# Performance work log

Hardware: AMD Instinct MI355X
Metric: run time of the kernel (lower is better)

The kernel has to match this reference:

```python
import jax, jax.numpy as jnp
import numpy as np

HIDDEN = 1024
NUM_EXPERTS = 8
TOP_K = 2
BATCH, SEQ = 4, 2048


def setup_inputs() -> dict:
    key = jax.random.key(0)
    ks = jax.random.split(key, 7)
    s = 0.02
    x = jax.random.normal(ks[0], (BATCH, SEQ, HIDDEN), dtype=jnp.float32)
    Wr = jax.random.normal(ks[1], (HIDDEN, NUM_EXPERTS), dtype=jnp.float32) * s
    br = jnp.zeros((NUM_EXPERTS,), dtype=jnp.float32)
    W1 = jax.random.normal(ks[2], (NUM_EXPERTS, HIDDEN, 2 * HIDDEN), dtype=jnp.float32) * s
    b1 = jnp.zeros((NUM_EXPERTS, 2 * HIDDEN), dtype=jnp.float32)
    W2 = jax.random.normal(ks[3], (NUM_EXPERTS, 2 * HIDDEN, HIDDEN), dtype=jnp.float32) * s
    b2 = jnp.zeros((NUM_EXPERTS, HIDDEN), dtype=jnp.float32)
    return {"x": x, "Wr": Wr, "br": br, "W1": W1, "b1": b1, "W2": W2, "b2": b2}


def reference(x, Wr, br, W1, b1, W2, b2):
    # Router: softmax over experts, take top-k, renormalize top-k weights.
    logits = jnp.einsum('bsh,he->bse', x, Wr) + br              # [B,S,E]
    routing = jax.nn.softmax(logits, axis=-1)
    topw, topi = jax.lax.top_k(routing, TOP_K)                   # [B,S,K]
    topw = jax.nn.softmax(topw, axis=-1)
    # Dense all-expert MLP (same math as masked gather/scatter combine).
    h = jnp.einsum('bsh,ehf->bsef', x, W1) + b1                  # [B,S,E,2H]
    h = jax.nn.gelu(h, approximate=False)                        # torch GELU = exact erf
    y = jnp.einsum('bsef,efh->bseh', h, W2) + b2                 # [B,S,E,H]
    # Per-token expert combine weights: sum_k onehot(topi_k)*topw_k -> [B,S,E]
    scale = jnp.sum(jax.nn.one_hot(topi, NUM_EXPERTS, dtype=x.dtype) * topw[..., None], axis=-2)
    return jnp.einsum('bse,bseh->bsh', scale, y)
```

## Files before the change

kernel.cpp:

```cpp
#include <hip/hip_runtime.h>
#include <math.h>

#define HID 1024
#define FF  2048
#define NE  8
#define NT  8192
#define MAXTILE 160

typedef __attribute__((ext_vector_type(4))) float f32x4;
typedef __bf16 bf16x8 __attribute__((ext_vector_type(8)));

#define GLL(g, l) __builtin_amdgcn_global_load_lds( \
    (const __attribute__((address_space(1))) unsigned int*)(g), \
    (__attribute__((address_space(3))) unsigned int*)(l), 16, 0, 0)

static __device__ __forceinline__ ushort f2b(float f){
  union { float f; unsigned int u; } v; v.f = f;
  unsigned int r = (v.u + 0x7FFFu + ((v.u >> 16) & 1u)) >> 16;
  return (ushort)r;
}

__global__ __launch_bounds__(256) void k_cvt_x(const float* __restrict__ x,
                                               ushort* __restrict__ xb){
  size_t i8 = ((size_t)blockIdx.x * 256 + threadIdx.x) * 8;
  const float* s = x + i8;
  ushort o[8];
  #pragma unroll
  for (int j = 0; j < 8; ++j) o[j] = f2b(s[j]);
  *(uint4*)(xb + i8) = *(uint4*)o;
}

__global__ __launch_bounds__(256) void k_transpose(
    const float* __restrict__ src, ushort* __restrict__ dst, int K, int N){
  __shared__ __align__(16) ushort Tt[64][72];
  int e = blockIdx.z;
  int n0 = blockIdx.x * 64, k0 = blockIdx.y * 64;
  int t = threadIdx.x;
  int r = t >> 2, c = (t & 3) * 16;
  const float* s = src + (size_t)e*K*N + (size_t)(k0+r)*N + n0 + c;
  #pragma unroll
  for (int q = 0; q < 4; ++q){
    float4 v = *(const float4*)(s + q*4);
    Tt[r][c+q*4+0] = f2b(v.x); Tt[r][c+q*4+1] = f2b(v.y);
    Tt[r][c+q*4+2] = f2b(v.z); Tt[r][c+q*4+3] = f2b(v.w);
  }
  __syncthreads();
  ushort tmp[16];
  #pragma unroll
  for (int i = 0; i < 16; ++i) tmp[i] = Tt[c+i][r];
  ushort* d = dst + (size_t)e*N*K + (size_t)(n0+r)*K + k0 + c;
  *(uint4*)(d)     = *(uint4*)&tmp[0];
  *(uint4*)(d + 8) = *(uint4*)&tmp[8];
}

__global__ __launch_bounds__(256) void k_router(
    const float* __restrict__ x, const float* __restrict__ Wr,
    const float* __restrict__ br, int* __restrict__ topi,
    float* __restrict__ topw){
  __shared__ __align__(16) float sW[HID*NE];
  int tid = threadIdx.x;
  const uint4* srcW = (const uint4*)Wr;
  uint4* dstW = (uint4*)sW;
  #pragma unroll
  for (int i = 0; i < 8; ++i) dstW[tid*8+i] = srcW[tid*8+i];
  __syncthreads();
  int wave = tid >> 6, lane = tid & 63;
  int t = blockIdx.x * 4 + wave;
  const float* xrow = x + (size_t)t * HID;
  double acc[NE];
  #pragma unroll
  for (int e=0;e<NE;++e) acc[e]=0.0;
  for (int it = 0; it < HID/64; ++it){
    int h = it*64 + lane;
    double xv = (double)xrow[h];
    #pragma unroll
    for (int e=0;e<NE;++e) acc[e] += xv * (double)sW[h*NE+e];
  }
  #pragma unroll
  for (int off=32; off>0; off>>=1){
    #pragma unroll
    for (int e=0;e<NE;++e) acc[e] += __shfl_down(acc[e], off, 64);
  }
  if (lane == 0){
    double lg[NE], p[NE];
    double m = -1e300;
    #pragma unroll
    for (int e=0;e<NE;++e){ lg[e] = acc[e] + (double)br[e]; m = fmax(m, lg[e]); }
    double s = 0.0;
    #pragma unroll
    for (int e=0;e<NE;++e){ p[e] = exp(lg[e]-m); s += p[e]; }
    double inv = 1.0 / s;
    #pragma unroll
    for (int e=0;e<NE;++e) p[e] *= inv;
    int i0 = 0;
    #pragma unroll
    for (int e=1;e<NE;++e) if (p[e] > p[i0]) i0 = e;
    int i1 = -1;
    #pragma unroll
    for (int e=0;e<NE;++e){ if (e==i0) continue; if (i1 < 0 || p[e] > p[i1]) i1 = e; }
    double d = exp(p[i1] - p[i0]);
    topi[t*2+0] = i0; topi[t*2+1] = i1;
    topw[t*2+0] = (float)(1.0 / (1.0 + d));
    topw[t*2+1] = (float)(d / (1.0 + d));
  }
}

__global__ __launch_bounds__(256) void k_count(
    const int* __restrict__ topi, int* __restrict__ counts){
  __shared__ int lcnt[NE];
  int tid = threadIdx.x;
  if (tid < NE) lcnt[tid] = 0;
  __syncthreads();
  int t = blockIdx.x * 256 + tid;
  atomicAdd(&lcnt[topi[t*2+0]], 1);
  atomicAdd(&lcnt[topi[t*2+1]], 1);
  __syncthreads();
  if (tid < NE) atomicAdd(&counts[tid], lcnt[tid]);
}

__global__ void k_offsets(const int* __restrict__ counts, int* __restrict__ offsets,
                          int* __restrict__ cursor, int* __restrict__ tile_e,
                          int* __restrict__ tile_m, int* __restrict__ ntiles){
  if (threadIdx.x == 0 && blockIdx.x == 0){
    int run = 0, nt = 0;
    for (int e=0;e<NE;++e){
      offsets[e] = run; cursor[e] = run;
      for (int m0 = 0; m0 < counts[e]; m0 += 128){ tile_e[nt] = e; tile_m[nt] = m0; ++nt; }
      run += counts[e];
    }
    *ntiles = nt;
  }
}

__global__ __launch_bounds__(256) void k_fill(
    const int* __restrict__ topi, const float* __restrict__ topw, int* __restrict__ cursor,
    int* __restrict__ tok_of, float* __restrict__ w_of){
  __shared__ int lcnt[NE];
  __shared__ int lbase[NE];
  int tid = threadIdx.x;
  if (tid < NE) lcnt[tid] = 0;
  __syncthreads();
  int t = blockIdx.x * 256 + tid;
  int e0 = topi[t*2+0], e1 = topi[t*2+1];
  int p0 = atomicAdd(&lcnt[e0], 1);
  int p1 = atomicAdd(&lcnt[e1], 1);
  __syncthreads();
  if (tid < NE) lbase[tid] = atomicAdd(&cursor[tid], lcnt[tid]);
  __syncthreads();
  int pos0 = lbase[e0] + p0;
  tok_of[pos0] = t; w_of[pos0] = topw[t*2+0];
  int pos1 = lbase[e1] + p1;
  tok_of[pos1] = t; w_of[pos1] = topw[t*2+1];
}

__global__ __launch_bounds__(256) void k_gemm1(
    const ushort* __restrict__ x, const ushort* __restrict__ w1t, const float* __restrict__ b1,
    const int* __restrict__ tok_of, const int* __restrict__ offsets, const int* __restrict__ counts,
    const int* __restrict__ tile_e, const int* __restrict__ tile_m, const int* __restrict__ ntiles,
    ushort* __restrict__ hbuf){
  int ty = blockIdx.y;
  if (ty >= *ntiles) return;
  int e = tile_e[ty];
  int m0 = tile_m[ty];
  int cnt = counts[e];
  int base = offsets[e];
  int n0 = blockIdx.x * 128;
  __shared__ __align__(16) ushort As[2][128][32];
  __shared__ __align__(16) ushort Bs[2][128][32];
  int tid = threadIdx.x;
  int wave = tid >> 6, lane = tid & 63;
  int srow0 = wave*32 + (lane >> 2);
  int srow1 = srow0 + 16;
  int chunk = (lane & 3) * 8;
  int t0 = tok_of[base + min(m0 + srow0, cnt-1)];
  int t1 = tok_of[base + min(m0 + srow1, cnt-1)];
  const ushort* agp0 = x + (size_t)t0*HID + chunk;
  const ushort* agp1 = x + (size_t)t1*HID + chunk;
  const ushort* wb = w1t + (size_t)e*FF*HID;
  const ushort* bgp0 = wb + (size_t)(n0 + srow0)*HID + chunk;
  const ushort* bgp1 = wb + (size_t)(n0 + srow1)*HID + chunk;
  f32x4 acc[4][4];
  #pragma unroll
  for (int i=0;i<4;++i)
    #pragma unroll
    for (int j=0;j<4;++j){ acc[i][j][0]=0.f; acc[i][j][1]=0.f; acc[i][j][2]=0.f; acc[i][j][3]=0.f; }
  int wr = (wave >> 1) * 64, wc = (wave & 1) * 64;
  int lrow = lane & 15, quad = lane >> 4;
  GLL(agp0, &As[0][wave*32][0]);
  GLL(agp1, &As[0][wave*32+16][0]);
  GLL(bgp0, &Bs[0][wave*32][0]);
  GLL(bgp1, &Bs[0][wave*32+16][0]);
  int cur = 0;
  for (int kk = 0; kk < HID; kk += 32){
    __syncthreads();
    int nxt = cur ^ 1;
    if (kk + 32 < HID){
      GLL(agp0 + kk + 32, &As[nxt][wave*32][0]);
      GLL(agp1 + kk + 32, &As[nxt][wave*32+16][0]);
      GLL(bgp0 + kk + 32, &Bs[nxt][wave*32][0]);
      GLL(bgp1 + kk + 32, &Bs[nxt][wave*32+16][0]);
    }
    bf16x8 af[4], bfr[4];
    #pragma unroll
    for (int i=0;i<4;++i) af[i]  = *(const bf16x8*)&As[cur][wr + i*16 + lrow][quad*8];
    #pragma unroll
    for (int j=0;j<4;++j) bfr[j] = *(const bf16x8*)&Bs[cur][wc + j*16 + lrow][quad*8];
    #pragma unroll
    for (int i=0;i<4;++i)
      #pragma unroll
      for (int j=0;j<4;++j)
        acc[i][j] = __builtin_amdgcn_mfma_f32_16x16x32_bf16(af[i], bfr[j], acc[i][j], 0, 0, 0);
    cur = nxt;
  }
  #pragma unroll
  for (int i=0;i<4;++i){
    #pragma unroll
    for (int rr=0; rr<4; ++rr){
      int mrel = wr + i*16 + quad*4 + rr;
      if (m0 + mrel < cnt){
        size_t grow = (size_t)(base + m0 + mrel) * FF;
        #pragma unroll
        for (int j=0;j<4;++j){
          int n = n0 + wc + j*16 + lrow;
          float v = acc[i][j][rr] + b1[e*FF + n];
          float g = 0.5f * v * (1.0f + erff(v * 0.70710678118654752f));
          hbuf[grow + n] = f2b(g);
        }
      }
    }
  }
}

__global__ __launch_bounds__(256) void k_gemm2(
    const ushort* __restrict__ hbuf, const ushort* __restrict__ w2t, const float* __restrict__ b2,
    const int* __restrict__ tok_of, const float* __restrict__ w_of,
    const int* __restrict__ offsets, const int* __restrict__ counts,
    const int* __restrict__ tile_e, const int* __restrict__ tile_m, const int* __restrict__ ntiles,
    float* __restrict__ outp){
  int ty = blockIdx.y;
  if (ty >= *ntiles) return;
  int e = tile_e[ty];
  int m0 = tile_m[ty];
  int cnt = counts[e];
  int base = offsets[e];
  int n0 = blockIdx.x * 128;
  __shared__ __align__(16) ushort As[2][128][32];
  __shared__ __align__(16) ushort Bs[2][128][32];
  int tid = threadIdx.x;
  int wave = tid >> 6, lane = tid & 63;
  int srow0 = wave*32 + (lane >> 2);
  int srow1 = srow0 + 16;
  int chunk = (lane & 3) * 8;
  int ar0 = base + min(m0 + srow0, cnt-1);
  int ar1 = base + min(m0 + srow1, cnt-1);
  const ushort* agp0 = hbuf + (size_t)ar0*FF + chunk;
  const ushort* agp1 = hbuf + (size_t)ar1*FF + chunk;
  const ushort* wb = w2t + (size_t)e*HID*FF;
  const ushort* bgp0 = wb + (size_t)(n0 + srow0)*FF + chunk;
  const ushort* bgp1 = wb + (size_t)(n0 + srow1)*FF + chunk;
  f32x4 acc[4][4];
  #pragma unroll
  for (int i=0;i<4;++i)
    #pragma unroll
    for (int j=0;j<4;++j){ acc[i][j][0]=0.f; acc[i][j][1]=0.f; acc[i][j][2]=0.f; acc[i][j][3]=0.f; }
  int wr = (wave >> 1) * 64, wc = (wave & 1) * 64;
  int lrow = lane & 15, quad = lane >> 4;
  GLL(agp0, &As[0][wave*32][0]);
  GLL(agp1, &As[0][wave*32+16][0]);
  GLL(bgp0, &Bs[0][wave*32][0]);
  GLL(bgp1, &Bs[0][wave*32+16][0]);
  int cur = 0;
  for (int kk = 0; kk < FF; kk += 32){
    __syncthreads();
    int nxt = cur ^ 1;
    if (kk + 32 < FF){
      GLL(agp0 + kk + 32, &As[nxt][wave*32][0]);
      GLL(agp1 + kk + 32, &As[nxt][wave*32+16][0]);
      GLL(bgp0 + kk + 32, &Bs[nxt][wave*32][0]);
      GLL(bgp1 + kk + 32, &Bs[nxt][wave*32+16][0]);
    }
    bf16x8 af[4], bfr[4];
    #pragma unroll
    for (int i=0;i<4;++i) af[i]  = *(const bf16x8*)&As[cur][wr + i*16 + lrow][quad*8];
    #pragma unroll
    for (int j=0;j<4;++j) bfr[j] = *(const bf16x8*)&Bs[cur][wc + j*16 + lrow][quad*8];
    #pragma unroll
    for (int i=0;i<4;++i)
      #pragma unroll
      for (int j=0;j<4;++j)
        acc[i][j] = __builtin_amdgcn_mfma_f32_16x16x32_bf16(af[i], bfr[j], acc[i][j], 0, 0, 0);
    cur = nxt;
  }
  #pragma unroll
  for (int i=0;i<4;++i){
    #pragma unroll
    for (int rr=0; rr<4; ++rr){
      int mrel = wr + i*16 + quad*4 + rr;
      if (m0 + mrel < cnt){
        int pos = base + m0 + mrel;
        int tok = tok_of[pos];
        float wgt = w_of[pos];
        float* orow = outp + (size_t)tok * HID;
        #pragma unroll
        for (int j=0;j<4;++j){
          int n = n0 + wc + j*16 + lrow;
          float y = acc[i][j][rr] + b2[e*HID + n];
          atomicAdd(&orow[n], wgt * y);
        }
      }
    }
  }
}

extern "C" void kernel_launch(void* const* d_in, const int* in_sizes, int n_in,
                              void* d_out, int out_size, void* d_ws, size_t ws_size,
                              hipStream_t stream) {
  const float* x  = (const float*)d_in[0];
  const float* Wr = (const float*)d_in[1];
  const float* br = (const float*)d_in[2];
  const float* W1 = (const float*)d_in[3];
  const float* b1 = (const float*)d_in[4];
  const float* W2 = (const float*)d_in[5];
  const float* b2 = (const float*)d_in[6];
  float* out = (float*)d_out;

  char* w = (char*)d_ws;
  int*   counts  = (int*)(w + 0);
  int*   cursor  = (int*)(w + 64);
  int*   offsets = (int*)(w + 128);
  int*   ntiles  = (int*)(w + 192);
  int*   tile_e  = (int*)(w + 1024);
  int*   tile_m  = (int*)(w + 1024 + MAXTILE*4);
  int*   topi    = (int*)(w + 131072);
  float* topw    = (float*)(w + 196608);
  int*   tok_of  = (int*)(w + 262144);
  float* w_of    = (float*)(w + 327680);
  const size_t XB_OFF  = 524288ull;
  const size_t W1T_OFF = XB_OFF  + 16ull*1024*1024;
  const size_t W2T_OFF = W1T_OFF + 32ull*1024*1024;
  const size_t HB_OFF  = W2T_OFF + 32ull*1024*1024;
  ushort* xb   = (ushort*)(w + XB_OFF);
  ushort* W1t  = (ushort*)(w + W1T_OFF);
  ushort* W2t  = (ushort*)(w + W2T_OFF);
  ushort* hbuf = (ushort*)(w + HB_OFF);

  hipMemsetAsync(w, 0, 256, stream);
  hipMemsetAsync(out, 0, (size_t)NT*HID*sizeof(float), stream);

  k_cvt_x<<<4096, 256, 0, stream>>>(x, xb);
  k_transpose<<<dim3(FF/64, HID/64, NE), 256, 0, stream>>>(W1, W1t, HID, FF);
  k_transpose<<<dim3(HID/64, FF/64, NE), 256, 0, stream>>>(W2, W2t, FF, HID);

  k_router<<<NT/4, 256, 0, stream>>>(x, Wr, br, topi, topw);
  k_count<<<NT/256, 256, 0, stream>>>(topi, counts);
  k_offsets<<<1, 64, 0, stream>>>(counts, offsets, cursor, tile_e, tile_m, ntiles);
  k_fill<<<NT/256, 256, 0, stream>>>(topi, topw, cursor, tok_of, w_of);

  k_gemm1<<<dim3(FF/128, MAXTILE), 256, 0, stream>>>(xb, W1t, b1, tok_of, offsets, counts,
                                                     tile_e, tile_m, ntiles, hbuf);
  k_gemm2<<<dim3(HID/128, MAXTILE), 256, 0, stream>>>(hbuf, W2t, b2, tok_of, w_of, offsets, counts,
                                                      tile_e, tile_m, ntiles, out);
}
```

Before: 568.0 us.

## Fuse x conversion into router, merge routing plan kernels, split-K gemm2, restructure gemm loads

Folds the x-to-bf16 conversion into the router kernel and replaces the count/offsets/fill kernels and a memset with a single-block plan kernel that uses wave ballots. gemm1 now loads 64-wide K chunks into both buffers per iteration, with barriers before and after compute, instead of double-buffered prefetch. gemm2 is split along K into two halves via a z grid dimension and accumulates atomically, and uses single-buffered loads. The aim is fewer launches and more parallelism in gemm2, at the cost of a serial single-block plan, lost load/compute overlap, and twice as many output atomics.

```diff
diff --git a/kernel.cpp b/kernel.cpp
--- a/kernel.cpp
+++ b/kernel.cpp
@@ -18,16 +18,6 @@
   union { float f; unsigned int u; } v; v.f = f;
   unsigned int r = (v.u + 0x7FFFu + ((v.u >> 16) & 1u)) >> 16;
   return (ushort)r;
-}
-
-__global__ __launch_bounds__(256) void k_cvt_x(const float* __restrict__ x,
-                                               ushort* __restrict__ xb){
-  size_t i8 = ((size_t)blockIdx.x * 256 + threadIdx.x) * 8;
-  const float* s = x + i8;
-  ushort o[8];
-  #pragma unroll
-  for (int j = 0; j < 8; ++j) o[j] = f2b(s[j]);
-  *(uint4*)(xb + i8) = *(uint4*)o;
 }
 
 __global__ __launch_bounds__(256) void k_transpose(
@@ -56,13 +46,23 @@
 __global__ __launch_bounds__(256) void k_router(
     const float* __restrict__ x, const float* __restrict__ Wr,
     const float* __restrict__ br, int* __restrict__ topi,
-    float* __restrict__ topw){
+    float* __restrict__ topw, ushort* __restrict__ xb){
   __shared__ __align__(16) float sW[HID*NE];
   int tid = threadIdx.x;
   const uint4* srcW = (const uint4*)Wr;
   uint4* dstW = (uint4*)sW;
   #pragma unroll
   for (int i = 0; i < 8; ++i) dstW[tid*8+i] = srcW[tid*8+i];
+
+  {
+    size_t base = (size_t)blockIdx.x * 4 * HID + (size_t)tid * 16;
+    const float* xs = x + base;
+    ushort o[16];
+    #pragma unroll
+    for (int j = 0; j < 16; ++j) o[j] = f2b(xs[j]);
+    *(uint4*)(xb + base)     = *(uint4*)&o[0];
+    *(uint4*)(xb + base + 8) = *(uint4*)&o[8];
+  }
   __syncthreads();
   int wave = tid >> 6, lane = tid & 63;
   int t = blockIdx.x * 4 + wave;
@@ -105,52 +105,54 @@
   }
 }
 
-__global__ __launch_bounds__(256) void k_count(
-    const int* __restrict__ topi, int* __restrict__ counts){
-  __shared__ int lcnt[NE];
-  int tid = threadIdx.x;
-  if (tid < NE) lcnt[tid] = 0;
-  __syncthreads();
-  int t = blockIdx.x * 256 + tid;
-  atomicAdd(&lcnt[topi[t*2+0]], 1);
-  atomicAdd(&lcnt[topi[t*2+1]], 1);
-  __syncthreads();
-  if (tid < NE) atomicAdd(&counts[tid], lcnt[tid]);
-}
-
-__global__ void k_offsets(const int* __restrict__ counts, int* __restrict__ offsets,
-                          int* __restrict__ cursor, int* __restrict__ tile_e,
-                          int* __restrict__ tile_m, int* __restrict__ ntiles){
-  if (threadIdx.x == 0 && blockIdx.x == 0){
+__global__ __launch_bounds__(256) void k_plan(
+    const int* __restrict__ topi, const float* __restrict__ topw,
+    int* __restrict__ counts, int* __restrict__ offsets,
+    int* __restrict__ tile_e, int* __restrict__ tile_m, int* __restrict__ ntiles,
+    int* __restrict__ tok_of, float* __restrict__ w_of){
+  __shared__ int cnt[NE];
+  __shared__ int cur[NE];
+  int tid = threadIdx.x, lane = tid & 63;
+  unsigned long long lt = (1ull << lane) - 1ull;
+  int myCnt = 0;
+  for (int idx = tid; idx < 2*NT; idx += 256){
+    int e = topi[idx];
+    #pragma unroll
+    for (int ee = 0; ee < NE; ++ee){
+      unsigned long long m = __ballot(e == ee);
+      if (lane == ee) myCnt += __popcll(m);
+    }
+  }
+  if (tid < NE) cnt[tid] = 0;
+  __syncthreads();
+  if (lane < NE) atomicAdd(&cnt[lane], myCnt);
+  __syncthreads();
+  if (tid == 0){
     int run = 0, nt = 0;
-    for (int e=0;e<NE;++e){
-      offsets[e] = run; cursor[e] = run;
-      for (int m0 = 0; m0 < counts[e]; m0 += 128){ tile_e[nt] = e; tile_m[nt] = m0; ++nt; }
-      run += counts[e];
+    for (int e = 0; e < NE; ++e){
+      int c = cnt[e];
+      counts[e] = c; offsets[e] = run; cur[e] = run;
+      for (int m0 = 0; m0 < c; m0 += 128){ tile_e[nt] = e; tile_m[nt] = m0; ++nt; }
+      run += c;
     }
     *ntiles = nt;
   }
-}
-
-__global__ __launch_bounds__(256) void k_fill(
-    const int* __restrict__ topi, const float* __restrict__ topw, int* __restrict__ cursor,
-    int* __restrict__ tok_of, float* __restrict__ w_of){
-  __shared__ int lcnt[NE];
-  __shared__ int lbase[NE];
-  int tid = threadIdx.x;
-  if (tid < NE) lcnt[tid] = 0;
-  __syncthreads();
-  int t = blockIdx.x * 256 + tid;
-  int e0 = topi[t*2+0], e1 = topi[t*2+1];
-  int p0 = atomicAdd(&lcnt[e0], 1);
-  int p1 = atomicAdd(&lcnt[e1], 1);
-  __syncthreads();
-  if (tid < NE) lbase[tid] = atomicAdd(&cursor[tid], lcnt[tid]);
-  __syncthreads();
-  int pos0 = lbase[e0] + p0;
-  tok_of[pos0] = t; w_of[pos0] = topw[t*2+0];
-  int pos1 = lbase[e1] + p1;
-  tok_of[pos1] = t; w_of[pos1] = topw[t*2+1];
+  __syncthreads();
+  for (int idx = tid; idx < 2*NT; idx += 256){
+    int e = topi[idx];
+    int pos = 0;
+    #pragma unroll
+    for (int ee = 0; ee < NE; ++ee){
+      unsigned long long m = __ballot(e == ee);
+      int c = __popcll(m);
+      int b = 0;
+      if (lane == ee && c) b = atomicAdd(&cur[ee], c);
+      b = __shfl(b, ee, 64);
+      if (e == ee) pos = b + (int)__popcll(m & lt);
+    }
+    tok_of[pos] = idx >> 1;
+    w_of[pos] = topw[idx];
+  }
 }
 
 __global__ __launch_bounds__(256) void k_gemm1(
@@ -186,31 +188,30 @@
     for (int j=0;j<4;++j){ acc[i][j][0]=0.f; acc[i][j][1]=0.f; acc[i][j][2]=0.f; acc[i][j][3]=0.f; }
   int wr = (wave >> 1) * 64, wc = (wave & 1) * 64;
   int lrow = lane & 15, quad = lane >> 4;
-  GLL(agp0, &As[0][wave*32][0]);
-  GLL(agp1, &As[0][wave*32+16][0]);
-  GLL(bgp0, &Bs[0][wave*32][0]);
-  GLL(bgp1, &Bs[0][wave*32+16][0]);
-  int cur = 0;
-  for (int kk = 0; kk < HID; kk += 32){
+  for (int kk = 0; kk < HID; kk += 64){
+    GLL(agp0 + kk,      &As[0][wave*32][0]);
+    GLL(agp1 + kk,      &As[0][wave*32+16][0]);
+    GLL(agp0 + kk + 32, &As[1][wave*32][0]);
+    GLL(agp1 + kk + 32, &As[1][wave*32+16][0]);
+    GLL(bgp0 + kk,      &Bs[0][wave*32][0]);
+    GLL(bgp1 + kk,      &Bs[0][wave*32+16][0]);
+    GLL(bgp0 + kk + 32, &Bs[1][wave*32][0]);
+    GLL(bgp1 + kk + 32, &Bs[1][wave*32+16][0]);
     __syncthreads();
-    int nxt = cur ^ 1;
-    if (kk + 32 < HID){
-      GLL(agp0 + kk + 32, &As[nxt][wave*32][0]);
-      GLL(agp1 + kk + 32, &As[nxt][wave*32+16][0]);
-      GLL(bgp0 + kk + 32, &Bs[nxt][wave*32][0]);
-      GLL(bgp1 + kk + 32, &Bs[nxt][wave*32+16][0]);
-    }
-    bf16x8 af[4], bfr[4];
-    #pragma unroll
-    for (int i=0;i<4;++i) af[i]  = *(const bf16x8*)&As[cur][wr + i*16 + lrow][quad*8];
-    #pragma unroll
-    for (int j=0;j<4;++j) bfr[j] = *(const bf16x8*)&Bs[cur][wc + j*16 + lrow][quad*8];
-    #pragma unroll
-    for (int i=0;i<4;++i)
+    #pragma unroll
+    for (int ko = 0; ko < 2; ++ko){
+      bf16x8 af[4], bfr[4];
       #pragma unroll
-      for (int j=0;j<4;++j)
-        acc[i][j] = __builtin_amdgcn_mfma_f32_16x16x32_bf16(af[i], bfr[j], acc[i][j], 0, 0, 0);
-    cur = nxt;
+      for (int i=0;i<4;++i) af[i]  = *(const bf16x8*)&As[ko][wr + i*16 + lrow][quad*8];
+      #pragma unroll
+      for (int j=0;j<4;++j) bfr[j] = *(const bf16x8*)&Bs[ko][wc + j*16 + lrow][quad*8];
+      #pragma unroll
+      for (int i=0;i<4;++i)
+        #pragma unroll
+        for (int j=0;j<4;++j)
+          acc[i][j] = __builtin_amdgcn_mfma_f32_16x16x32_bf16(af[i], bfr[j], acc[i][j], 0, 0, 0);
+    }
+    __syncthreads();
   }
   #pragma unroll
   for (int i=0;i<4;++i){
@@ -244,8 +245,10 @@
   int cnt = counts[e];
   int base = offsets[e];
   int n0 = blockIdx.x * 128;
-  __shared__ __align__(16) ushort As[2][128][32];
-  __shared__ __align__(16) ushort Bs[2][128][32];
+  int kz = blockIdx.z;
+  const int KH = FF/2;
+  __shared__ __align__(16) ushort As[128][32];
+  __shared__ __align__(16) ushort Bs[128][32];
   int tid = threadIdx.x;
   int wave = tid >> 6, lane = tid & 63;
   int srow0 = wave*32 + (lane >> 2);
@@ -253,11 +256,11 @@
   int chunk = (lane & 3) * 8;
   int ar0 = base + min(m0 + srow0, cnt-1);
   int ar1 = base + min(m0 + srow1, cnt-1);
-  const ushort* agp0 = hbuf + (size_t)ar0*FF + chunk;
-  const ushort* agp1 = hbuf + (size_t)ar1*FF + chunk;
+  const ushort* agp0 = hbuf + (size_t)ar0*FF + kz*KH + chunk;
+  const ushort* agp1 = hbuf + (size_t)ar1*FF + kz*KH + chunk;
   const ushort* wb = w2t + (size_t)e*HID*FF;
-  const ushort* bgp0 = wb + (size_t)(n0 + srow0)*FF + chunk;
-  const ushort* bgp1 = wb + (size_t)(n0 + srow1)*FF + chunk;
+  const ushort* bgp0 = wb + (size_t)(n0 + srow0)*FF + kz*KH + chunk;
+  const ushort* bgp1 = wb + (size_t)(n0 + srow1)*FF + kz*KH + chunk;
   f32x4 acc[4][4];
   #pragma unroll
   for (int i=0;i<4;++i)
@@ -265,31 +268,23 @@
     for (int j=0;j<4;++j){ acc[i][j][0]=0.f; acc[i][j][1]=0.f; acc[i][j][2]=0.f; acc[i][j][3]=0.f; }
   int wr = (wave >> 1) * 64, wc = (wave & 1) * 64;
   int lrow = lane & 15, quad = lane >> 4;
-  GLL(agp0, &As[0][wave*32][0]);
-  GLL(agp1, &As[0][wave*32+16][0]);
-  GLL(bgp0, &Bs[0][wave*32][0]);
-  GLL(bgp1, &Bs[0][wave*32+16][0]);
-  int cur = 0;
-  for (int kk = 0; kk < FF; kk += 32){
+  for (int kk = 0; kk < KH; kk += 32){
+    GLL(agp0 + kk, &As[wave*32][0]);
+    GLL(agp1 + kk, &As[wave*32+16][0]);
+    GLL(bgp0 + kk, &Bs[wave*32][0]);
+    GLL(bgp1 + kk, &Bs[wave*32+16][0]);
     __syncthreads();
-    int nxt = cur ^ 1;
-    if (kk + 32 < FF){
-      GLL(agp0 + kk + 32, &As[nxt][wave*32][0]);
-      GLL(agp1 + kk + 32, &As[nxt][wave*32+16][0]);
-      GLL(bgp0 + kk + 32, &Bs[nxt][wave*32][0]);
-      GLL(bgp1 + kk + 32, &Bs[nxt][wave*32+16][0]);
-    }
     bf16x8 af[4], bfr[4];
     #pragma unroll
-    for (int i=0;i<4;++i) af[i]  = *(const bf16x8*)&As[cur][wr + i*16 + lrow][quad*8];
-    #pragma unroll
-    for (int j=0;j<4;++j) bfr[j] = *(const bf16x8*)&Bs[cur][wc + j*16 + lrow][quad*8];
+    for (int i=0;i<4;++i) af[i]  = *(const bf16x8*)&As[wr + i*16 + lrow][quad*8];
+    #pragma unroll
+    for (int j=0;j<4;++j) bfr[j] = *(const bf16x8*)&Bs[wc + j*16 + lrow][quad*8];
     #pragma unroll
     for (int i=0;i<4;++i)
       #pragma unroll
       for (int j=0;j<4;++j)
         acc[i][j] = __builtin_amdgcn_mfma_f32_16x16x32_bf16(af[i], bfr[j], acc[i][j], 0, 0, 0);
-    cur = nxt;
+    __syncthreads();
   }
   #pragma unroll
   for (int i=0;i<4;++i){
@@ -304,7 +299,7 @@
         #pragma unroll
         for (int j=0;j<4;++j){
           int n = n0 + wc + j*16 + lrow;
-          float y = acc[i][j][rr] + b2[e*HID + n];
+          float y = acc[i][j][rr] + (kz == 0 ? b2[e*HID + n] : 0.f);
           atomicAdd(&orow[n], wgt * y);
         }
       }
@@ -326,9 +321,8 @@
 
   char* w = (char*)d_ws;
   int*   counts  = (int*)(w + 0);
-  int*   cursor  = (int*)(w + 64);
-  int*   offsets = (int*)(w + 128);
-  int*   ntiles  = (int*)(w + 192);
+  int*   offsets = (int*)(w + 64);
+  int*   ntiles  = (int*)(w + 128);
   int*   tile_e  = (int*)(w + 1024);
   int*   tile_m  = (int*)(w + 1024 + MAXTILE*4);
   int*   topi    = (int*)(w + 131072);
@@ -344,20 +338,15 @@
   ushort* W2t  = (ushort*)(w + W2T_OFF);
   ushort* hbuf = (ushort*)(w + HB_OFF);
 
-  hipMemsetAsync(w, 0, 256, stream);
   hipMemsetAsync(out, 0, (size_t)NT*HID*sizeof(float), stream);
 
-  k_cvt_x<<<4096, 256, 0, stream>>>(x, xb);
+  k_router<<<NT/4, 256, 0, stream>>>(x, Wr, br, topi, topw, xb);
   k_transpose<<<dim3(FF/64, HID/64, NE), 256, 0, stream>>>(W1, W1t, HID, FF);
   k_transpose<<<dim3(HID/64, FF/64, NE), 256, 0, stream>>>(W2, W2t, FF, HID);
-
-  k_router<<<NT/4, 256, 0, stream>>>(x, Wr, br, topi, topw);
-  k_count<<<NT/256, 256, 0, stream>>>(topi, counts);
-  k_offsets<<<1, 64, 0, stream>>>(counts, offsets, cursor, tile_e, tile_m, ntiles);
-  k_fill<<<NT/256, 256, 0, stream>>>(topi, topw, cursor, tok_of, w_of);
+  k_plan<<<1, 256, 0, stream>>>(topi, topw, counts, offsets, tile_e, tile_m, ntiles, tok_of, w_of);
 
   k_gemm1<<<dim3(FF/128, MAXTILE), 256, 0, stream>>>(xb, W1t, b1, tok_of, offsets, counts,
                                                      tile_e, tile_m, ntiles, hbuf);
-  k_gemm2<<<dim3(HID/128, MAXTILE), 256, 0, stream>>>(hbuf, W2t, b2, tok_of, w_of, offsets, counts,
-                                                      tile_e, tile_m, ntiles, out);
-}
+  k_gemm2<<<dim3(HID/128, MAXTILE, 2), 256, 0, stream>>>(hbuf, W2t, b2, tok_of, w_of, offsets, counts,
+                                                         tile_e, tile_m, ntiles, out);
+}
```

Measured after the change: 678.3 us. 1.19x slower.
